# Kernel optimization log

Measured on AMD Instinct MI355X. Metric: run time of the kernel, lower is better.

Reference implementation:

```python
import jax, jax.numpy as jnp
import numpy as np

B, S, D_MODEL, HEADS = 2, 2048, 1024, 16
K_D = D_MODEL // HEADS


def setup_inputs() -> dict:
    key = jax.random.key(0)
    ks = jax.random.split(key, 5)
    x = jax.random.normal(ks[0], (B, S, D_MODEL), dtype=jnp.float32)
    # causal mask, 1 = keep, 0 = masked (GPT-2 style)
    mask = jnp.tril(jnp.ones((S, S), dtype=jnp.int32))[None, None, :, :]
    sc = 0.02
    w_attn = jax.random.normal(ks[1], (D_MODEL, 3 * D_MODEL), dtype=jnp.float32) * sc
    b_attn = jax.random.normal(ks[2], (3 * D_MODEL,), dtype=jnp.float32) * sc
    w_proj = jax.random.normal(ks[3], (D_MODEL, D_MODEL), dtype=jnp.float32) * sc
    b_proj = jax.random.normal(ks[4], (D_MODEL,), dtype=jnp.float32) * sc
    return {"x": x, "mask": mask, "w_attn": w_attn, "b_attn": b_attn,
            "w_proj": w_proj, "b_proj": b_proj}


def reference(x, mask, w_attn, b_attn, w_proj, b_proj):
    b, s, _ = x.shape
    qkv = x @ w_attn + b_attn                      # [B,S,3*d_model]
    # NOTE: source assigns value, query, key = split(...) in that order
    v, q, k = jnp.split(qkv, 3, axis=-1)
    def heads(t):  # [B,S,d_model] -> [B,H,S,k_d]
        return t.reshape(b, s, HEADS, K_D).transpose(0, 2, 1, 3)
    v, q, k = heads(v), heads(q), heads(k)
    present = jnp.stack((k, v))                    # [2,B,H,S,k_d]
    scores = jnp.einsum('bhqd,bhkd->bhqk', q, k) / jnp.sqrt(jnp.float32(K_D))
    scores = jnp.where(mask == 0, -jnp.inf, scores)
    attn = jax.nn.softmax(scores, axis=-1)         # [B,H,S,S]
    out = jnp.einsum('bhqk,bhkd->bhqd', attn, v)   # [B,H,S,k_d]
    out = out.transpose(0, 2, 1, 3).reshape(b, s, D_MODEL)
    out = out @ w_proj + b_proj
    return out, present
```

## Files before the change

kernel.cpp:

```cpp
#include <hip/hip_runtime.h>
#include <math.h>

constexpr int BB = 2;
constexpr int SS = 2048;
constexpr int DM = 1024;
constexpr int NH = 16;
constexpr int KD = 64;
constexpr int OUT_ELEMS  = BB*SS*DM;
constexpr int PRES_HALF  = BB*NH*SS*KD;
#define NEGSENT (-1e30f)

typedef __attribute__((ext_vector_type(8))) short short8;
typedef __attribute__((ext_vector_type(4))) short short4v;
typedef __attribute__((ext_vector_type(4))) float f32x4;

__device__ __forceinline__ float us2f(unsigned short u) {
  union { unsigned int ui; float f; } c; c.ui = ((unsigned int)u) << 16; return c.f;
}
__device__ __forceinline__ short f2s(float f) {
  union { float f; unsigned int u; } c; c.f = f;
  return (short)((c.u + 0x7FFFu + ((c.u >> 16) & 1u)) >> 16);
}

#define GLOAD_LDS16(g, l) \
  __builtin_amdgcn_global_load_lds((const __attribute__((address_space(1))) void*)(g), \
                                   (__attribute__((address_space(3))) void*)(l), 16, 0, 0)

__global__ __launch_bounds__(256)
void cast_x_k(const float* __restrict__ x, short* __restrict__ xb) {
  const size_t i = ((size_t)blockIdx.x * 256 + threadIdx.x) * 4;
  const float4 v = *(const float4*)(x + i);
  short4v s; s.x = f2s(v.x); s.y = f2s(v.y); s.z = f2s(v.z); s.w = f2s(v.w);
  *(short4v*)(xb + i) = s;
}

__global__ __launch_bounds__(256)
void transpose_k(const float* __restrict__ w, int N, short* __restrict__ wt) {
  __shared__ float tl[32][33];
  const int tx = threadIdx.x & 31, ty = threadIdx.x >> 5;
  const int n0 = blockIdx.x * 32, k0 = blockIdx.y * 32;
  #pragma unroll
  for (int i = 0; i < 4; ++i) {
    const int kk = ty + i * 8;
    tl[kk][tx] = w[(size_t)(k0 + kk) * N + n0 + tx];
  }
  __syncthreads();
  #pragma unroll
  for (int i = 0; i < 4; ++i) {
    const int nn = ty + i * 8;
    wt[(size_t)(n0 + nn) * 1024 + k0 + tx] = f2s(tl[tx][nn]);
  }
}

__device__ __forceinline__ void mfma_tile_loop(
    const short* __restrict__ A, const short* __restrict__ Bt,
    int m0, int n0, short* Asm, short* Bsm, f32x4 (*acc)[4]) {
  const int tid = threadIdx.x;
  const int lane = tid & 63;
  const int w = tid >> 6;
  const int wm = (w >> 1) * 64, wn = (w & 1) * 64;
  const int ln15 = lane & 15, quad = lane >> 4;
  for (int k0 = 0; k0 < 1024; k0 += 64) {
    #pragma unroll
    for (int j = 0; j < 4; ++j) {
      const int e = j * 256 + tid;
      const int r = e >> 3, cq = e & 7;
      GLOAD_LDS16(A  + (size_t)(m0 + r) * 1024 + k0 + cq * 8, Asm + e * 8);
      GLOAD_LDS16(Bt + (size_t)(n0 + r) * 1024 + k0 + cq * 8, Bsm + e * 8);
    }
    __syncthreads();
    #pragma unroll
    for (int kk = 0; kk < 2; ++kk) {
      short8 af[4], bf[4];
      #pragma unroll
      for (int t = 0; t < 4; ++t)
        af[t] = *(const short8*)(Asm + (wm + t * 16 + ln15) * 64 + kk * 32 + quad * 8);
      #pragma unroll
      for (int t = 0; t < 4; ++t)
        bf[t] = *(const short8*)(Bsm + (wn + t * 16 + ln15) * 64 + kk * 32 + quad * 8);
      #pragma unroll
      for (int tm = 0; tm < 4; ++tm)
        #pragma unroll
        for (int tn = 0; tn < 4; ++tn)
          acc[tm][tn] = __builtin_amdgcn_mfma_f32_16x16x32_bf16(
              af[tm], bf[tn], acc[tm][tn], 0, 0, 0);
    }
    __syncthreads();
  }
}

__global__ __launch_bounds__(256)
void qkv_mfma_k(const short* __restrict__ A, const short* __restrict__ Bt,
                const float* __restrict__ bias, short* __restrict__ qbf,
                float* __restrict__ outf, short* __restrict__ kbf,
                short* __restrict__ vbft) {
  __shared__ short Asm[128 * 64];
  __shared__ short Bsm[128 * 64];
  const int n0 = blockIdx.x * 128, m0 = blockIdx.y * 128;
  f32x4 acc[4][4] = {};
  mfma_tile_loop(A, Bt, m0, n0, Asm, Bsm, acc);
  const int lane = threadIdx.x & 63;
  const int w = threadIdx.x >> 6;
  const int wm = (w >> 1) * 64, wn = (w & 1) * 64;
  const int col = lane & 15, row4 = (lane >> 4) * 4;
  #pragma unroll
  for (int tm = 0; tm < 4; ++tm) {
    #pragma unroll
    for (int tn = 0; tn < 4; ++tn) {
      const int n = n0 + wn + tn * 16 + col;
      #pragma unroll
      for (int r = 0; r < 4; ++r) {
        const int m = m0 + wm + tm * 16 + row4 + r;
        const float val = acc[tm][tn][r] + bias[n];
        const int bb = m >> 11, s = m & 2047;
        const int c = n & 1023, h = c >> 6, d = c & 63;
        const size_t idx = ((size_t)(bb * NH + h) * SS + s) * KD + d;
        if (n < DM) {
          outf[(size_t)OUT_ELEMS + (size_t)PRES_HALF + idx] = val;
          if (kbf) vbft[((size_t)(bb * NH + h) * KD + d) * SS + s] = f2s(val);
        } else if (n < 2 * DM) {
          qbf[idx] = f2s(val);
        } else {
          outf[(size_t)OUT_ELEMS + idx] = val;
          if (kbf) kbf[idx] = f2s(val);
        }
      }
    }
  }
}

__global__ __launch_bounds__(256)
void proj_mfma_k(const short* __restrict__ A, const short* __restrict__ Bt,
                 const float* __restrict__ bias, float* __restrict__ outf) {
  __shared__ short Asm[128 * 64];
  __shared__ short Bsm[128 * 64];
  const int n0 = blockIdx.x * 128, m0 = blockIdx.y * 128;
  f32x4 acc[4][4] = {};
  mfma_tile_loop(A, Bt, m0, n0, Asm, Bsm, acc);
  const int lane = threadIdx.x & 63;
  const int w = threadIdx.x >> 6;
  const int wm = (w >> 1) * 64, wn = (w & 1) * 64;
  const int col = lane & 15, row4 = (lane >> 4) * 4;
  #pragma unroll
  for (int tm = 0; tm < 4; ++tm) {
    #pragma unroll
    for (int tn = 0; tn < 4; ++tn) {
      const int n = n0 + wn + tn * 16 + col;
      const float b = bias[n];
      #pragma unroll
      for (int r = 0; r < 4; ++r) {
        const int m = m0 + wm + tm * 16 + row4 + r;
        outf[(size_t)m * DM + n] = acc[tm][tn][r] + b;
      }
    }
  }
}

__device__ __forceinline__ void stage_kv4(const short* __restrict__ Kg,
                                          const short* __restrict__ Vg,
                                          int kb, short* Ksb, short* Vtb,
                                          int tid) {
  #pragma unroll
  for (int rd = 0; rd < 2; ++rd) {
    const int i = rd * 256 + tid;
    const int row = i >> 3, grp = i & 7;
    const int sw = (grp ^ (row & 7)) << 3;
    GLOAD_LDS16(Kg + (size_t)(kb + row) * KD + sw, Ksb + i * 8);
    GLOAD_LDS16(Vg + (size_t)row * SS + kb + sw, Vtb + i * 8);
  }
}

__global__ __launch_bounds__(256)
void attn_mfma6_k(const short* __restrict__ qbf, const short* __restrict__ kbf,
                  const short* __restrict__ vbft, short* __restrict__ obf) {
  __shared__ short Ks[2][64 * 64];
  __shared__ short Vt[2][64 * 64];
  __shared__ short Ps[4][16 * 64];
  const int bid = blockIdx.x;
  const int xcd = bid & 7, g = bid >> 3;
  const int rr  = g & 31, rnd = g >> 5;
  const int bh  = (xcd << 2) | rnd;
  const int qb  = (rnd & 1) ? rr : 31 - rr;
  const int q0  = qb * 64;
  const int tid = threadIdx.x;
  const int w   = tid >> 6;
  const int lane = tid & 63;
  const int ln15 = lane & 15, quad = lane >> 4;
  const int rswz = (ln15 & 7) << 3;
  const float SC2 = 0.125f * 1.44269504f;
  const float THR = 8.0f;

  short8 aq[2];
  {
    const short* qp = qbf + ((size_t)bh * SS + q0 + w * 16) * KD;
    aq[0] = *(const short8*)(qp + (size_t)ln15 * KD + quad * 8);
    aq[1] = *(const short8*)(qp + (size_t)ln15 * KD + 32 + quad * 8);
  }
  f32x4 O[4] = {};
  float mreg[4], lreg[4];
  #pragma unroll
  for (int r = 0; r < 4; ++r) { mreg[r] = NEGSENT; lreg[r] = 0.f; }

  const short* Kg = kbf  + (size_t)bh * SS * KD;
  const short* Vg = vbft + (size_t)bh * KD * SS;
  short* Pw = Ps[w];
  const int nch = qb + 1;

  stage_kv4(Kg, Vg, 0, Ks[0], Vt[0], tid);
  __syncthreads();

  for (int ch = 0; ch < nch; ++ch) {
    const int cur = ch & 1;
    if (ch + 1 < nch)
      stage_kv4(Kg, Vg, (ch + 1) * 64, Ks[cur ^ 1], Vt[cur ^ 1], tid);
    const short* Kc = Ks[cur];
    const short* Vc = Vt[cur];

    f32x4 S[4] = {};
    #pragma unroll
    for (int kt = 0; kt < 2; ++kt) {
      short8 bk[4];
      #pragma unroll
      for (int tn = 0; tn < 4; ++tn)
        bk[tn] = *(const short8*)(Kc + (tn * 16 + ln15) * 64 + ((kt * 32 + quad * 8) ^ rswz));
      #pragma unroll
      for (int tn = 0; tn < 4; ++tn)
        S[tn] = __builtin_amdgcn_mfma_f32_16x16x32_bf16(aq[kt], bk[tn], S[tn], 0, 0, 0);
    }

    if (ch == qb) {
      const int rowl = w * 16 + quad * 4;
      #pragma unroll
      for (int tn = 0; tn < 4; ++tn) {
        const int colk = tn * 16 + ln15;
        #pragma unroll
        for (int r = 0; r < 4; ++r)
          if (colk > rowl + r) S[tn][r] = NEGSENT;
      }
    }

    float pmax[4];
    #pragma unroll
    for (int r = 0; r < 4; ++r) {
      float mx = fmaxf(fmaxf(fmaxf(S[0][r], S[1][r]), S[2][r]), S[3][r]);
      mx = fmaxf(mx, __shfl_xor(mx, 1, 64));
      mx = fmaxf(mx, __shfl_xor(mx, 2, 64));
      mx = fmaxf(mx, __shfl_xor(mx, 4, 64));
      mx = fmaxf(mx, __shfl_xor(mx, 8, 64));
      pmax[r] = mx;
    }

    bool okl = true;
    #pragma unroll
    for (int r = 0; r < 4; ++r) okl = okl && (pmax[r] - mreg[r] <= THR);
    if (!__all((int)okl)) {
      #pragma unroll
      for (int r = 0; r < 4; ++r) {
        const float mn = fmaxf(mreg[r], pmax[r]);
        const float al = exp2f((mreg[r] - mn) * SC2);
        mreg[r] = mn;
        lreg[r] *= al;
        O[0][r] *= al; O[1][r] *= al; O[2][r] *= al; O[3][r] *= al;
      }
    }

    #pragma unroll
    for (int r = 0; r < 4; ++r) {
      const float mnsc = mreg[r] * SC2;
      const int prow = quad * 4 + r;
      const int rs = (prow & 7) << 3;
      float p0 = exp2f(fmaf(S[0][r], SC2, -mnsc));
      float p1 = exp2f(fmaf(S[1][r], SC2, -mnsc));
      float p2 = exp2f(fmaf(S[2][r], SC2, -mnsc));
      float p3 = exp2f(fmaf(S[3][r], SC2, -mnsc));
      lreg[r] += (p0 + p1) + (p2 + p3);
      Pw[prow * 64 + ((0 * 16 + ln15) ^ rs)] = f2s(p0);
      Pw[prow * 64 + ((1 * 16 + ln15) ^ rs)] = f2s(p1);
      Pw[prow * 64 + ((2 * 16 + ln15) ^ rs)] = f2s(p2);
      Pw[prow * 64 + ((3 * 16 + ln15) ^ rs)] = f2s(p3);
    }
    asm volatile("s_waitcnt lgkmcnt(0)" ::: "memory");
    __builtin_amdgcn_sched_barrier(0);

    #pragma unroll
    for (int kt = 0; kt < 2; ++kt) {
      short8 ap = *(const short8*)(Pw + ln15 * 64 + ((kt * 32 + quad * 8) ^ rswz));
      short8 bv[4];
      #pragma unroll
      for (int tn = 0; tn < 4; ++tn)
        bv[tn] = *(const short8*)(Vc + (tn * 16 + ln15) * 64 + ((kt * 32 + quad * 8) ^ rswz));
      #pragma unroll
      for (int tn = 0; tn < 4; ++tn)
        O[tn] = __builtin_amdgcn_mfma_f32_16x16x32_bf16(ap, bv[tn], O[tn], 0, 0, 0);
    }
    __syncthreads();
  }

  #pragma unroll
  for (int r = 0; r < 4; ++r) {
    float l = lreg[r];
    l += __shfl_xor(l, 1, 64);
    l += __shfl_xor(l, 2, 64);
    l += __shfl_xor(l, 4, 64);
    l += __shfl_xor(l, 8, 64);
    lreg[r] = 1.f / fmaxf(l, 1e-30f);
  }
  const int bb = bh >> 4, h = bh & 15;
  short* ob = obf + ((size_t)bb * SS + q0 + w * 16) * DM + h * KD;
  #pragma unroll
  for (int tn = 0; tn < 4; ++tn)
    #pragma unroll
    for (int r = 0; r < 4; ++r)
      ob[(size_t)(quad * 4 + r) * DM + tn * 16 + ln15] = f2s(O[tn][r] * lreg[r]);
}

__global__ __launch_bounds__(256)
void attn_k(const short* __restrict__ qbf, const float* __restrict__ pres,
            short* __restrict__ obf) {
  __shared__ float Ksf[32][64];
  __shared__ float Vsf[32][64];
  const int bh = blockIdx.x;
  const int q0 = ((int)gridDim.y - 1 - (int)blockIdx.y) * 64;
  const int t  = threadIdx.x;
  const int part = t & 3;
  const int row  = t >> 2;
  const int qr   = q0 + row;
  const int dbase = part * 16;
  const size_t qoff = ((size_t)bh * SS + qr) * KD + dbase;
  float q[16], o[16];
  #pragma unroll
  for (int i = 0; i < 16; ++i) q[i] = us2f((unsigned short)qbf[qoff + i]);
  #pragma unroll
  for (int i = 0; i < 16; ++i) o[i] = 0.f;
  float m = NEGSENT, l = 0.f;
  const float* Kb = pres + (size_t)bh * SS * KD;
  const float* Vb = pres + (size_t)PRES_HALF + (size_t)bh * SS * KD;
  const int nch = (q0 + 64) / 32;
  for (int ch = 0; ch < nch; ++ch) {
    const int kbase = ch * 32;
    __syncthreads();
    {
      const float4* ksrc = (const float4*)(Kb + (size_t)kbase * KD);
      const float4* vsrc = (const float4*)(Vb + (size_t)kbase * KD);
      float4* kdst = (float4*)&Ksf[0][0];
      float4* vdst = (float4*)&Vsf[0][0];
      #pragma unroll
      for (int i = 0; i < 2; ++i) {
        kdst[t + i * 256] = ksrc[t + i * 256];
        vdst[t + i * 256] = vsrc[t + i * 256];
      }
    }
    __syncthreads();
    float sc[32];
    #pragma unroll
    for (int kk = 0; kk < 32; ++kk) {
      float s = 0.f;
      #pragma unroll
      for (int i = 0; i < 16; ++i) s = fmaf(q[i], Ksf[kk][dbase + i], s);
      s += __shfl_xor(s, 1, 64);
      s += __shfl_xor(s, 2, 64);
      sc[kk] = (kbase + kk <= qr) ? s * 0.125f : NEGSENT;
    }
    float mc = sc[0];
    #pragma unroll
    for (int kk = 1; kk < 32; ++kk) mc = fmaxf(mc, sc[kk]);
    const float mn = fmaxf(m, mc);
    const float alpha = __expf(m - mn);
    l *= alpha;
    #pragma unroll
    for (int i = 0; i < 16; ++i) o[i] *= alpha;
    #pragma unroll
    for (int kk = 0; kk < 32; ++kk) {
      const float p = __expf(sc[kk] - mn);
      l += p;
      #pragma unroll
      for (int i = 0; i < 16; ++i) o[i] = fmaf(p, Vsf[kk][dbase + i], o[i]);
    }
    m = mn;
  }
  const float inv = 1.f / fmaxf(l, 1e-30f);
  const int bb = bh >> 4, h = bh & 15;
  const size_t ooff = ((size_t)(bb * SS + qr)) * DM + h * KD + dbase;
  #pragma unroll
  for (int i = 0; i < 16; ++i) obf[ooff + i] = f2s(o[i] * inv);
}

extern "C" void kernel_launch(void* const* d_in, const int* in_sizes, int n_in,
                              void* d_out, int out_size, void* d_ws, size_t ws_size,
                              hipStream_t stream) {
  const float* x      = (const float*)d_in[0];
  const float* w_attn = (const float*)d_in[2];
  const float* b_attn = (const float*)d_in[3];
  const float* w_proj = (const float*)d_in[4];
  const float* b_proj = (const float*)d_in[5];
  float* outf = (float*)d_out;

  constexpr size_t MB = 1024 * 1024;
  if (ws_size >= 24 * MB) {
    short* ws0   = (short*)d_ws;
    short* x_bf  = ws0;
    short* o_bf  = ws0;
    short* wat_t = ws0 + (size_t)4 * 1024 * 1024;
    short* wpt_t = ws0 + (size_t)7 * 1024 * 1024;
    short* q_bf  = ws0 + (size_t)8 * 1024 * 1024;
    short* k_bf  = (short*)d_out;
    short* v_bft = k_bf + (size_t)PRES_HALF;

    cast_x_k<<<4096, 256, 0, stream>>>(x, x_bf);
    transpose_k<<<dim3(96, 32), 256, 0, stream>>>(w_attn, 3 * DM, wat_t);
    transpose_k<<<dim3(32, 32), 256, 0, stream>>>(w_proj, DM, wpt_t);

    qkv_mfma_k<<<dim3(24, 32), 256, 0, stream>>>(x_bf, wat_t, b_attn, q_bf, outf,
                                                 k_bf, v_bft);

    attn_mfma6_k<<<dim3(BB * NH * (SS / 64)), 256, 0, stream>>>(q_bf, k_bf, v_bft, o_bf);

    proj_mfma_k<<<dim3(8, 32), 256, 0, stream>>>(o_bf, wpt_t, b_proj, outf);
  } else {
    short* x_bf;
    short* q_bf;
    short* wat_t;
    short* wpt_t;
    short* o_bf;
    if (ws_size >= 16 * MB) {
      short* ws = (short*)d_ws;
      x_bf  = (short*)d_out;
      q_bf  = x_bf + OUT_ELEMS;
      wat_t = ws;
      wpt_t = wat_t + 3 * DM * DM;
      o_bf  = wat_t + 4 * DM * DM;
    } else {
      x_bf  = (short*)d_out;
      q_bf  = x_bf + OUT_ELEMS;
      wat_t = (short*)d_in[1];
      wpt_t = wat_t + 3 * DM * DM;
      o_bf  = wat_t + 4 * DM * DM;
    }
    cast_x_k<<<4096, 256, 0, stream>>>(x, x_bf);
    transpose_k<<<dim3(96, 32), 256, 0, stream>>>(w_attn, 3 * DM, wat_t);
    transpose_k<<<dim3(32, 32), 256, 0, stream>>>(w_proj, DM, wpt_t);
    qkv_mfma_k<<<dim3(24, 32), 256, 0, stream>>>(x_bf, wat_t, b_attn, q_bf, outf,
                                                 nullptr, nullptr);
    attn_k<<<dim3(BB * NH, SS / 64), 256, 0, stream>>>(q_bf, outf + OUT_ELEMS, o_bf);
    proj_mfma_k<<<dim3(8, 32), 256, 0, stream>>>(o_bf, wpt_t, b_proj, outf);
  }
}
```

Before: 261.9 us.

## Pair causal query blocks per CTA, split V transpose out, shrink GEMM k-tile

Attention blocks now each process two query blocks (p and 31-p) so every block does equal causal work, halving the grid. The transposed bf16 V copy is no longer written with scattered strided stores in the QKV GEMM epilogue; a separate LDS-tiled transpose kernel builds it from the fp32 present buffer. The shared GEMM loop uses a 32-wide k-step, halving shared memory per block, at the cost of more barriers per tile. The extra kernel launch and re-read of V add traffic.

```diff
diff --git a/kernel.cpp b/kernel.cpp
--- a/kernel.cpp
+++ b/kernel.cpp
@@ -52,6 +52,31 @@
   }
 }
 
+__global__ __launch_bounds__(256)
+void v_tr_k(const float* __restrict__ vf, short* __restrict__ vt) {
+  __shared__ float tl[64][65];
+  const int bh = blockIdx.x;
+  const int s0 = blockIdx.y * 64;
+  const int tr = threadIdx.x >> 2;
+  const int tc = (threadIdx.x & 3) * 16;
+  const float* src = vf + ((size_t)bh * SS + s0) * KD;
+  #pragma unroll
+  for (int i = 0; i < 4; ++i) {
+    const float4 v = *(const float4*)(src + (size_t)tr * KD + tc + i * 4);
+    tl[tr][tc + i * 4 + 0] = v.x; tl[tr][tc + i * 4 + 1] = v.y;
+    tl[tr][tc + i * 4 + 2] = v.z; tl[tr][tc + i * 4 + 3] = v.w;
+  }
+  __syncthreads();
+  short8 o0, o1;
+  #pragma unroll
+  for (int i = 0; i < 8; ++i) o0[i] = f2s(tl[tc + i][tr]);
+  #pragma unroll
+  for (int i = 0; i < 8; ++i) o1[i] = f2s(tl[tc + 8 + i][tr]);
+  short* dst = vt + ((size_t)bh * KD + tr) * SS + s0 + tc;
+  *(short8*)(dst) = o0;
+  *(short8*)(dst + 8) = o1;
+}
+
 __device__ __forceinline__ void mfma_tile_loop(
     const short* __restrict__ A, const short* __restrict__ Bt,
     int m0, int n0, short* Asm, short* Bsm, f32x4 (*acc)[4]) {
@@ -60,31 +85,28 @@
   const int w = tid >> 6;
   const int wm = (w >> 1) * 64, wn = (w & 1) * 64;
   const int ln15 = lane & 15, quad = lane >> 4;
-  for (int k0 = 0; k0 < 1024; k0 += 64) {
-    #pragma unroll
-    for (int j = 0; j < 4; ++j) {
+  for (int k0 = 0; k0 < 1024; k0 += 32) {
+    #pragma unroll
+    for (int j = 0; j < 2; ++j) {
       const int e = j * 256 + tid;
-      const int r = e >> 3, cq = e & 7;
+      const int r = e >> 2, cq = e & 3;
       GLOAD_LDS16(A  + (size_t)(m0 + r) * 1024 + k0 + cq * 8, Asm + e * 8);
       GLOAD_LDS16(Bt + (size_t)(n0 + r) * 1024 + k0 + cq * 8, Bsm + e * 8);
     }
     __syncthreads();
-    #pragma unroll
-    for (int kk = 0; kk < 2; ++kk) {
-      short8 af[4], bf[4];
-      #pragma unroll
-      for (int t = 0; t < 4; ++t)
-        af[t] = *(const short8*)(Asm + (wm + t * 16 + ln15) * 64 + kk * 32 + quad * 8);
-      #pragma unroll
-      for (int t = 0; t < 4; ++t)
-        bf[t] = *(const short8*)(Bsm + (wn + t * 16 + ln15) * 64 + kk * 32 + quad * 8);
-      #pragma unroll
-      for (int tm = 0; tm < 4; ++tm)
-        #pragma unroll
-        for (int tn = 0; tn < 4; ++tn)
-          acc[tm][tn] = __builtin_amdgcn_mfma_f32_16x16x32_bf16(
-              af[tm], bf[tn], acc[tm][tn], 0, 0, 0);
-    }
+    short8 af[4], bf[4];
+    #pragma unroll
+    for (int t = 0; t < 4; ++t)
+      af[t] = *(const short8*)(Asm + (wm + t * 16 + ln15) * 32 + quad * 8);
+    #pragma unroll
+    for (int t = 0; t < 4; ++t)
+      bf[t] = *(const short8*)(Bsm + (wn + t * 16 + ln15) * 32 + quad * 8);
+    #pragma unroll
+    for (int tm = 0; tm < 4; ++tm)
+      #pragma unroll
+      for (int tn = 0; tn < 4; ++tn)
+        acc[tm][tn] = __builtin_amdgcn_mfma_f32_16x16x32_bf16(
+            af[tm], bf[tn], acc[tm][tn], 0, 0, 0);
     __syncthreads();
   }
 }
@@ -92,10 +114,9 @@
 __global__ __launch_bounds__(256)
 void qkv_mfma_k(const short* __restrict__ A, const short* __restrict__ Bt,
                 const float* __restrict__ bias, short* __restrict__ qbf,
-                float* __restrict__ outf, short* __restrict__ kbf,
-                short* __restrict__ vbft) {
-  __shared__ short Asm[128 * 64];
-  __shared__ short Bsm[128 * 64];
+                float* __restrict__ outf, short* __restrict__ kbf) {
+  __shared__ short Asm[128 * 32];
+  __shared__ short Bsm[128 * 32];
   const int n0 = blockIdx.x * 128, m0 = blockIdx.y * 128;
   f32x4 acc[4][4] = {};
   mfma_tile_loop(A, Bt, m0, n0, Asm, Bsm, acc);
@@ -117,7 +138,6 @@
         const size_t idx = ((size_t)(bb * NH + h) * SS + s) * KD + d;
         if (n < DM) {
           outf[(size_t)OUT_ELEMS + (size_t)PRES_HALF + idx] = val;
-          if (kbf) vbft[((size_t)(bb * NH + h) * KD + d) * SS + s] = f2s(val);
         } else if (n < 2 * DM) {
           qbf[idx] = f2s(val);
         } else {
@@ -132,8 +152,8 @@
 __global__ __launch_bounds__(256)
 void proj_mfma_k(const short* __restrict__ A, const short* __restrict__ Bt,
                  const float* __restrict__ bias, float* __restrict__ outf) {
-  __shared__ short Asm[128 * 64];
-  __shared__ short Bsm[128 * 64];
+  __shared__ short Asm[128 * 32];
+  __shared__ short Bsm[128 * 32];
   const int n0 = blockIdx.x * 128, m0 = blockIdx.y * 128;
   f32x4 acc[4][4] = {};
   mfma_tile_loop(A, Bt, m0, n0, Asm, Bsm, acc);
@@ -171,17 +191,16 @@
 }
 
 __global__ __launch_bounds__(256)
-void attn_mfma6_k(const short* __restrict__ qbf, const short* __restrict__ kbf,
+void attn_mfma7_k(const short* __restrict__ qbf, const short* __restrict__ kbf,
                   const short* __restrict__ vbft, short* __restrict__ obf) {
   __shared__ short Ks[2][64 * 64];
   __shared__ short Vt[2][64 * 64];
   __shared__ short Ps[4][16 * 64];
   const int bid = blockIdx.x;
   const int xcd = bid & 7, g = bid >> 3;
-  const int rr  = g & 31, rnd = g >> 5;
+  const int rnd = g >> 4;
+  const int p   = g & 15;
   const int bh  = (xcd << 2) | rnd;
-  const int qb  = (rnd & 1) ? rr : 31 - rr;
-  const int q0  = qb * 64;
   const int tid = threadIdx.x;
   const int w   = tid >> 6;
   const int lane = tid & 63;
@@ -190,128 +209,134 @@
   const float SC2 = 0.125f * 1.44269504f;
   const float THR = 8.0f;
 
-  short8 aq[2];
-  {
-    const short* qp = qbf + ((size_t)bh * SS + q0 + w * 16) * KD;
-    aq[0] = *(const short8*)(qp + (size_t)ln15 * KD + quad * 8);
-    aq[1] = *(const short8*)(qp + (size_t)ln15 * KD + 32 + quad * 8);
-  }
-  f32x4 O[4] = {};
-  float mreg[4], lreg[4];
-  #pragma unroll
-  for (int r = 0; r < 4; ++r) { mreg[r] = NEGSENT; lreg[r] = 0.f; }
-
   const short* Kg = kbf  + (size_t)bh * SS * KD;
   const short* Vg = vbft + (size_t)bh * KD * SS;
   short* Pw = Ps[w];
-  const int nch = qb + 1;
-
-  stage_kv4(Kg, Vg, 0, Ks[0], Vt[0], tid);
-  __syncthreads();
-
-  for (int ch = 0; ch < nch; ++ch) {
-    const int cur = ch & 1;
-    if (ch + 1 < nch)
-      stage_kv4(Kg, Vg, (ch + 1) * 64, Ks[cur ^ 1], Vt[cur ^ 1], tid);
-    const short* Kc = Ks[cur];
-    const short* Vc = Vt[cur];
-
-    f32x4 S[4] = {};
-    #pragma unroll
-    for (int kt = 0; kt < 2; ++kt) {
-      short8 bk[4];
-      #pragma unroll
-      for (int tn = 0; tn < 4; ++tn)
-        bk[tn] = *(const short8*)(Kc + (tn * 16 + ln15) * 64 + ((kt * 32 + quad * 8) ^ rswz));
-      #pragma unroll
-      for (int tn = 0; tn < 4; ++tn)
-        S[tn] = __builtin_amdgcn_mfma_f32_16x16x32_bf16(aq[kt], bk[tn], S[tn], 0, 0, 0);
-    }
-
-    if (ch == qb) {
-      const int rowl = w * 16 + quad * 4;
-      #pragma unroll
-      for (int tn = 0; tn < 4; ++tn) {
-        const int colk = tn * 16 + ln15;
-        #pragma unroll
-        for (int r = 0; r < 4; ++r)
-          if (colk > rowl + r) S[tn][r] = NEGSENT;
-      }
-    }
-
-    float pmax[4];
+  const int bb = bh >> 4, h = bh & 15;
+
+  #pragma unroll 1
+  for (int pass = 0; pass < 2; ++pass) {
+    const int qb = pass ? (31 - p) : p;
+    const int q0 = qb * 64;
+    const int nch = qb + 1;
+
+    short8 aq[2];
+    {
+      const short* qp = qbf + ((size_t)bh * SS + q0 + w * 16) * KD;
+      aq[0] = *(const short8*)(qp + (size_t)ln15 * KD + quad * 8);
+      aq[1] = *(const short8*)(qp + (size_t)ln15 * KD + 32 + quad * 8);
+    }
+    f32x4 O[4] = {};
+    float mreg[4], lreg[4];
+    #pragma unroll
+    for (int r = 0; r < 4; ++r) { mreg[r] = NEGSENT; lreg[r] = 0.f; }
+
+    stage_kv4(Kg, Vg, 0, Ks[0], Vt[0], tid);
+    __syncthreads();
+
+    for (int ch = 0; ch < nch; ++ch) {
+      const int cur = ch & 1;
+      if (ch + 1 < nch)
+        stage_kv4(Kg, Vg, (ch + 1) * 64, Ks[cur ^ 1], Vt[cur ^ 1], tid);
+      const short* Kc = Ks[cur];
+      const short* Vc = Vt[cur];
+
+      f32x4 S[4] = {};
+      #pragma unroll
+      for (int kt = 0; kt < 2; ++kt) {
+        short8 bk[4];
+        #pragma unroll
+        for (int tn = 0; tn < 4; ++tn)
+          bk[tn] = *(const short8*)(Kc + (tn * 16 + ln15) * 64 + ((kt * 32 + quad * 8) ^ rswz));
+        #pragma unroll
+        for (int tn = 0; tn < 4; ++tn)
+          S[tn] = __builtin_amdgcn_mfma_f32_16x16x32_bf16(aq[kt], bk[tn], S[tn], 0, 0, 0);
+      }
+
+      if (ch == qb) {
+        const int rowl = w * 16 + quad * 4;
+        #pragma unroll
+        for (int tn = 0; tn < 4; ++tn) {
+          const int colk = tn * 16 + ln15;
+          #pragma unroll
+          for (int r = 0; r < 4; ++r)
+            if (colk > rowl + r) S[tn][r] = NEGSENT;
+        }
+      }
+
+      float pmax[4];
+      #pragma unroll
+      for (int r = 0; r < 4; ++r) {
+        float mx = fmaxf(fmaxf(fmaxf(S[0][r], S[1][r]), S[2][r]), S[3][r]);
+        mx = fmaxf(mx, __shfl_xor(mx, 1, 64));
+        mx = fmaxf(mx, __shfl_xor(mx, 2, 64));
+        mx = fmaxf(mx, __shfl_xor(mx, 4, 64));
+        mx = fmaxf(mx, __shfl_xor(mx, 8, 64));
+        pmax[r] = mx;
+      }
+
+      bool okl = true;
+      #pragma unroll
+      for (int r = 0; r < 4; ++r) okl = okl && (pmax[r] - mreg[r] <= THR);
+      if (!__all((int)okl)) {
+        #pragma unroll
+        for (int r = 0; r < 4; ++r) {
+          const float mn = fmaxf(mreg[r], pmax[r]);
+          const float al = exp2f((mreg[r] - mn) * SC2);
+          mreg[r] = mn;
+          lreg[r] *= al;
+          O[0][r] *= al; O[1][r] *= al; O[2][r] *= al; O[3][r] *= al;
+        }
+      }
+
+      #pragma unroll
+      for (int r = 0; r < 4; ++r) {
+        const float mnsc = mreg[r] * SC2;
+        const int prow = quad * 4 + r;
+        const int rs = (prow & 7) << 3;
+        float p0 = exp2f(fmaf(S[0][r], SC2, -mnsc));
+        float p1 = exp2f(fmaf(S[1][r], SC2, -mnsc));
+        float p2 = exp2f(fmaf(S[2][r], SC2, -mnsc));
+        float p3 = exp2f(fmaf(S[3][r], SC2, -mnsc));
+        lreg[r] += (p0 + p1) + (p2 + p3);
+        Pw[prow * 64 + ((0 * 16 + ln15) ^ rs)] = f2s(p0);
+        Pw[prow * 64 + ((1 * 16 + ln15) ^ rs)] = f2s(p1);
+        Pw[prow * 64 + ((2 * 16 + ln15) ^ rs)] = f2s(p2);
+        Pw[prow * 64 + ((3 * 16 + ln15) ^ rs)] = f2s(p3);
+      }
+      asm volatile("s_waitcnt lgkmcnt(0)" ::: "memory");
+      __builtin_amdgcn_sched_barrier(0);
+
+      #pragma unroll
+      for (int kt = 0; kt < 2; ++kt) {
+        short8 ap = *(const short8*)(Pw + ln15 * 64 + ((kt * 32 + quad * 8) ^ rswz));
+        short8 bv[4];
+        #pragma unroll
+        for (int tn = 0; tn < 4; ++tn)
+          bv[tn] = *(const short8*)(Vc + (tn * 16 + ln15) * 64 + ((kt * 32 + quad * 8) ^ rswz));
+        #pragma unroll
+        for (int tn = 0; tn < 4; ++tn)
+          O[tn] = __builtin_amdgcn_mfma_f32_16x16x32_bf16(ap, bv[tn], O[tn], 0, 0, 0);
+      }
+      __syncthreads();
+    }
+
     #pragma unroll
     for (int r = 0; r < 4; ++r) {
-      float mx = fmaxf(fmaxf(fmaxf(S[0][r], S[1][r]), S[2][r]), S[3][r]);
-      mx = fmaxf(mx, __shfl_xor(mx, 1, 64));
-      mx = fmaxf(mx, __shfl_xor(mx, 2, 64));
-      mx = fmaxf(mx, __shfl_xor(mx, 4, 64));
-      mx = fmaxf(mx, __shfl_xor(mx, 8, 64));
-      pmax[r] = mx;
-    }
-
-    bool okl = true;
-    #pragma unroll
-    for (int r = 0; r < 4; ++r) okl = okl && (pmax[r] - mreg[r] <= THR);
-    if (!__all((int)okl)) {
-      #pragma unroll
-      for (int r = 0; r < 4; ++r) {
-        const float mn = fmaxf(mreg[r], pmax[r]);
-        const float al = exp2f((mreg[r] - mn) * SC2);
-        mreg[r] = mn;
-        lreg[r] *= al;
-        O[0][r] *= al; O[1][r] *= al; O[2][r] *= al; O[3][r] *= al;
-      }
-    }
-
-    #pragma unroll
-    for (int r = 0; r < 4; ++r) {
-      const float mnsc = mreg[r] * SC2;
-      const int prow = quad * 4 + r;
-      const int rs = (prow & 7) << 3;
-      float p0 = exp2f(fmaf(S[0][r], SC2, -mnsc));
-      float p1 = exp2f(fmaf(S[1][r], SC2, -mnsc));
-      float p2 = exp2f(fmaf(S[2][r], SC2, -mnsc));
-      float p3 = exp2f(fmaf(S[3][r], SC2, -mnsc));
-      lreg[r] += (p0 + p1) + (p2 + p3);
-      Pw[prow * 64 + ((0 * 16 + ln15) ^ rs)] = f2s(p0);
-      Pw[prow * 64 + ((1 * 16 + ln15) ^ rs)] = f2s(p1);
-      Pw[prow * 64 + ((2 * 16 + ln15) ^ rs)] = f2s(p2);
-      Pw[prow * 64 + ((3 * 16 + ln15) ^ rs)] = f2s(p3);
-    }
-    asm volatile("s_waitcnt lgkmcnt(0)" ::: "memory");
-    __builtin_amdgcn_sched_barrier(0);
-
-    #pragma unroll
-    for (int kt = 0; kt < 2; ++kt) {
-      short8 ap = *(const short8*)(Pw + ln15 * 64 + ((kt * 32 + quad * 8) ^ rswz));
-      short8 bv[4];
-      #pragma unroll
-      for (int tn = 0; tn < 4; ++tn)
-        bv[tn] = *(const short8*)(Vc + (tn * 16 + ln15) * 64 + ((kt * 32 + quad * 8) ^ rswz));
-      #pragma unroll
-      for (int tn = 0; tn < 4; ++tn)
-        O[tn] = __builtin_amdgcn_mfma_f32_16x16x32_bf16(ap, bv[tn], O[tn], 0, 0, 0);
-    }
-    __syncthreads();
-  }
-
-  #pragma unroll
-  for (int r = 0; r < 4; ++r) {
-    float l = lreg[r];
-    l += __shfl_xor(l, 1, 64);
-    l += __shfl_xor(l, 2, 64);
-    l += __shfl_xor(l, 4, 64);
-    l += __shfl_xor(l, 8, 64);
-    lreg[r] = 1.f / fmaxf(l, 1e-30f);
-  }
-  const int bb = bh >> 4, h = bh & 15;
-  short* ob = obf + ((size_t)bb * SS + q0 + w * 16) * DM + h * KD;
-  #pragma unroll
-  for (int tn = 0; tn < 4; ++tn)
-    #pragma unroll
-    for (int r = 0; r < 4; ++r)
-      ob[(size_t)(quad * 4 + r) * DM + tn * 16 + ln15] = f2s(O[tn][r] * lreg[r]);
+      float l = lreg[r];
+      l += __shfl_xor(l, 1, 64);
+      l += __shfl_xor(l, 2, 64);
+      l += __shfl_xor(l, 4, 64);
+      l += __shfl_xor(l, 8, 64);
+      lreg[r] = 1.f / fmaxf(l, 1e-30f);
+    }
+    short* ob = obf + ((size_t)bb * SS + q0 + w * 16) * DM + h * KD;
+    #pragma unroll
+    for (int tn = 0; tn < 4; ++tn)
+      #pragma unroll
+      for (int r = 0; r < 4; ++r)
+        ob[(size_t)(quad * 4 + r) * DM + tn * 16 + ln15] = f2s(O[tn][r] * lreg[r]);
+  }
 }
 
 __global__ __launch_bounds__(256)
@@ -411,9 +436,12 @@
     transpose_k<<<dim3(32, 32), 256, 0, stream>>>(w_proj, DM, wpt_t);
 
     qkv_mfma_k<<<dim3(24, 32), 256, 0, stream>>>(x_bf, wat_t, b_attn, q_bf, outf,
-                                                 k_bf, v_bft);
-
-    attn_mfma6_k<<<dim3(BB * NH * (SS / 64)), 256, 0, stream>>>(q_bf, k_bf, v_bft, o_bf);
+                                                 k_bf);
+
+    v_tr_k<<<dim3(BB * NH, SS / 64), 256, 0, stream>>>(
+        outf + OUT_ELEMS + PRES_HALF, v_bft);
+
+    attn_mfma7_k<<<dim3(512), 256, 0, stream>>>(q_bf, k_bf, v_bft, o_bf);
 
     proj_mfma_k<<<dim3(8, 32), 256, 0, stream>>>(o_bf, wpt_t, b_proj, outf);
   } else {
@@ -440,7 +468,7 @@
     transpose_k<<<dim3(96, 32), 256, 0, stream>>>(w_attn, 3 * DM, wat_t);
     transpose_k<<<dim3(32, 32), 256, 0, stream>>>(w_proj, DM, wpt_t);
     qkv_mfma_k<<<dim3(24, 32), 256, 0, stream>>>(x_bf, wat_t, b_attn, q_bf, outf,
-                                                 nullptr, nullptr);
+                                                 nullptr);
     attn_k<<<dim3(BB * NH, SS / 64), 256, 0, stream>>>(q_bf, outf + OUT_ELEMS, o_bf);
     proj_mfma_k<<<dim3(8, 32), 256, 0, stream>>>(o_bf, wpt_t, b_proj, outf);
   }
```

Result: faster. 236.2 us (-9.8%).
